# Optimization experiments

Measured on AMD Instinct MI355X. Metric: run time of the kernel, lower is better.

The kernel has to match this reference:

```python
import jax, jax.numpy as jnp
import numpy as np

E, N, D, H, K, S = 800000, 50000, 96, 8, 12, 32  # edges, nodes, dim, heads, head_dim, edge_scalar_dim


def smooth_leaky_relu(x, a=0.2):
    # equiformer SmoothLeakyReLU: (1+a)/2 * x + (1-a)/2 * x * (2*sigmoid(x) - 1)
    return ((1 + a) / 2) * x + ((1 - a) / 2) * x * (2 * jax.nn.sigmoid(x) - 1)


def setup_inputs() -> dict:
    key = jax.random.key(0)
    ks = jax.random.split(key, 16)
    inv = lambda n: 1.0 / np.sqrt(n)
    return {
        "message": jax.random.normal(ks[0], (E, D), jnp.float32),
        "edge_attr": jax.random.normal(ks[1], (E, 1), jnp.float32),
        "edge_scalars": jax.random.normal(ks[2], (E, S), jnp.float32),
        "W_rad1": jax.random.normal(ks[3], (S, S), jnp.float32) * inv(S),
        "b_rad1": jnp.zeros((S,), jnp.float32),
        "W_rad2": jax.random.normal(ks[4], (S, D), jnp.float32) * inv(S),
        "b_rad2": jnp.zeros((D,), jnp.float32),
        "W_alpha": jax.random.normal(ks[5], (D, D), jnp.float32) * inv(D),
        "W_lin": jax.random.normal(ks[6], (D, D), jnp.float32) * inv(D),
        "w_dtp2": jax.random.normal(ks[7], (D,), jnp.float32),
        "W_lin2": jax.random.normal(ks[8], (D, D), jnp.float32) * inv(D),
        "alpha_dot": jax.random.normal(ks[9], (H, K), jnp.float32) * inv(K),
        "W_proj": jax.random.normal(ks[10], (D, D), jnp.float32) * inv(D),
        "edge_dst": jnp.sort(jax.random.randint(ks[11], (E,), 0, N)),
        "n_nodes_dst": N,
    }


def reference(message, edge_attr, edge_scalars, W_rad1, b_rad1, W_rad2, b_rad2,
              W_alpha, W_lin, w_dtp2, W_lin2, alpha_dot, W_proj,
              edge_dst, n_nodes_dst):
    # sep_act.dtp_rad: radial MLP on edge scalars -> depthwise TP weights [E, D]
    weight = jax.nn.silu(edge_scalars @ W_rad1 + b_rad1) @ W_rad2 + b_rad2
    # sep_act.dtp: depthwise tensor product (scalar irreps -> per-channel product)
    msg = message * edge_attr * weight                      # [E, D]
    # sep_alpha: LinearRS to mul_alpha scalars, split into heads
    log_alpha = (msg @ W_alpha).reshape(E, H, K)            # [E, H, K]
    # sep_act.lin + gate (scalar gate == SiLU)
    value = jax.nn.silu(msg @ W_lin)                        # [E, D]
    # sep_value: internal-weight depthwise TP + linear
    value = (value * edge_attr * w_dtp2) @ W_lin2           # [E, D]
    # attention logits
    la = smooth_leaky_relu(log_alpha)
    logits = jnp.einsum('ehk,hk->eh', la, alpha_dot)        # [E, H]
    # scatter_logsumexp over destination nodes (segment softmax)
    m = jax.ops.segment_max(logits, edge_dst, num_segments=n_nodes_dst)     # [N, H]
    z = jax.ops.segment_sum(jnp.exp(logits - m[edge_dst]), edge_dst,
                            num_segments=n_nodes_dst)
    log_Z = m + jnp.log(z)                                  # [N, H]
    alpha = jnp.exp(logits - log_Z[edge_dst])               # [E, H]
    # weighted scatter-sum aggregation
    attn = jax.ops.segment_sum(value.reshape(E, H, K) * alpha[:, :, None],
                               edge_dst, num_segments=n_nodes_dst)          # [N, H, K]
    # heads2vec + proj
    return attn.reshape(n_nodes_dst, D) @ W_proj            # [N, D]
```

## Files before the change

kernel.cpp:

```cpp
#include <hip/hip_runtime.h>
#include <hip/hip_bf16.h>
#include <math.h>

#define D 96
#define H 8
#define KH 12
#define S 32

typedef __attribute__((ext_vector_type(8))) short short8;
typedef __attribute__((ext_vector_type(4))) float f32x4;

#define MFMA(a, b, c) __builtin_amdgcn_mfma_f32_16x16x32_bf16(a, b, c, 0, 0, 0)

__device__ __forceinline__ float sigmoidf_(float x) { return 1.0f / (1.0f + __expf(-x)); }
__device__ __forceinline__ float siluf_(float x) { return x * sigmoidf_(x); }
__device__ __forceinline__ float slrelu_(float x) {
    float s = sigmoidf_(x);
    return 0.6f * x + 0.4f * x * (2.0f * s - 1.0f);
}
__device__ __forceinline__ short f2bf(float f) {
    unsigned int u = __float_as_uint(f);
    u += 0x7fffu + ((u >> 16) & 1u);
    return (short)(u >> 16);
}
__device__ __forceinline__ float bf2f(ushort u) {
    return __uint_as_float(((unsigned int)u) << 16);
}

__global__ void pack_weights_kernel(
    const float* __restrict__ W1, const float* __restrict__ W2,
    const float* __restrict__ WA, const float* __restrict__ WL,
    const float* __restrict__ WL2, const float* __restrict__ WP,
    short* __restrict__ wB)
{
    int tid = blockIdx.x * 256 + threadIdx.x;
    if (tid >= 80 * 512) return;
    int j    = tid & 7;
    int lane = (tid >> 3) & 63;
    int fi   = tid >> 9;
    int q = lane >> 4, ln = lane & 15;
    const float* src; int ncols, tt, ff;
    if (fi < 2)       { src = W1;  ncols = 32; tt = fi;            ff = 0; }
    else if (fi < 8)  { src = W2;  ncols = 96; tt = fi - 2;        ff = 0; }
    else if (fi < 26) { src = WA;  ncols = 96; tt = (fi - 8) / 3;  ff = (fi - 8) % 3; }
    else if (fi < 44) { src = WL;  ncols = 96; tt = (fi - 26) / 3; ff = (fi - 26) % 3; }
    else if (fi < 62) { src = WL2; ncols = 96; tt = (fi - 44) / 3; ff = (fi - 44) % 3; }
    else              { src = WP;  ncols = 96; tt = (fi - 62) / 3; ff = (fi - 62) % 3; }
    int k = ff * 32 + q * 8 + j;
    int n = tt * 16 + ln;
    wB[tid] = f2bf(src[k * ncols + n]);
}

__global__ __launch_bounds__(256) void rowptr_kernel(
    const int* __restrict__ dst, int* __restrict__ rp, int E, int N)
{
    int e = blockIdx.x * 256 + threadIdx.x;
    if (e >= E) return;
    int cur  = dst[e];
    int prev = (e == 0) ? -1 : dst[e - 1];
    for (int n = prev + 1; n <= cur; n++) rp[n] = e;
    if (e == E - 1)
        for (int n = cur + 1; n <= N; n++) rp[n] = E;
}

__global__ __launch_bounds__(256, 6) void fused_edge_kernel(
    const float* __restrict__ message, const float* __restrict__ ea,
    const float* __restrict__ xs,
    const float* __restrict__ b1, const float* __restrict__ b2,
    const float* __restrict__ wdtp2, const float* __restrict__ adot,
    const short* __restrict__ wB,
    ushort* __restrict__ value, float* __restrict__ logits, int E)
{
    __shared__ __align__(16) char uni[64 * 97 * 4];
    short* sB = (short*)uni;
    float* sS = (float*)uni;
    const short8* wB8 = (const short8*)wB;

    const int t    = threadIdx.x;
    const int lane = t & 63;
    const int w    = t >> 6;
    const int q    = lane >> 4;
    const int ln   = lane & 15;
    const int row0 = blockIdx.x * 64;

    const int mA = w * 16 + ln;
    const int gA = row0 + mA;
    const int mC = w * 16 + q * 4;

    short8 af;
    {
        float4 x0 = make_float4(0, 0, 0, 0), x1 = x0;
        if (gA < E) {
            const float4* p = (const float4*)&xs[(size_t)gA * S + q * 8];
            x0 = p[0]; x1 = p[1];
        }
        af[0] = f2bf(x0.x); af[1] = f2bf(x0.y); af[2] = f2bf(x0.z); af[3] = f2bf(x0.w);
        af[4] = f2bf(x1.x); af[5] = f2bf(x1.y); af[6] = f2bf(x1.z); af[7] = f2bf(x1.w);
    }
    {
        f32x4 h0 = {0, 0, 0, 0}, h1 = {0, 0, 0, 0};
        h0 = MFMA(af, wB8[0 * 64 + lane], h0);
        h1 = MFMA(af, wB8[1 * 64 + lane], h1);
#pragma unroll
        for (int r = 0; r < 4; r++) {
            sB[(mC + r) * 104 + ln]      = f2bf(siluf_(h0[r] + b1[ln]));
            sB[(mC + r) * 104 + 16 + ln] = f2bf(siluf_(h1[r] + b1[16 + ln]));
        }
    }

    f32x4 acc[6];
    {
        short8 hf = *(const short8*)&sB[mA * 104 + q * 8];
#pragma unroll
        for (int i = 0; i < 6; i++) acc[i] = (f32x4){0, 0, 0, 0};
#pragma unroll
        for (int i = 0; i < 6; i++) acc[i] = MFMA(hf, wB8[(2 + i) * 64 + lane], acc[i]);
    }
    float eaR[4];
#pragma unroll
    for (int r = 0; r < 4; r++) {
        int gm = row0 + mC + r;
        eaR[r] = (gm < E) ? ea[gm] : 0.0f;
    }
#pragma unroll
    for (int i = 0; i < 6; i++) {
        int n = i * 16 + ln;
#pragma unroll
        for (int r = 0; r < 4; r++) {
            int gm = row0 + mC + r;
            float mv = (gm < E) ? message[(size_t)gm * D + n] : 0.0f;
            sB[(mC + r) * 104 + n] = f2bf(mv * eaR[r] * (acc[i][r] + b2[n]));
        }
    }

    short8 mf0 = *(const short8*)&sB[mA * 104 + 0  + q * 8];
    short8 mf1 = *(const short8*)&sB[mA * 104 + 32 + q * 8];
    short8 mf2 = *(const short8*)&sB[mA * 104 + 64 + q * 8];
    __syncthreads();

#pragma unroll
    for (int i = 0; i < 6; i++) acc[i] = (f32x4){0, 0, 0, 0};
#pragma unroll
    for (int i = 0; i < 6; i++) {
        acc[i] = MFMA(mf0, wB8[(8 + i * 3 + 0) * 64 + lane], acc[i]);
        acc[i] = MFMA(mf1, wB8[(8 + i * 3 + 1) * 64 + lane], acc[i]);
        acc[i] = MFMA(mf2, wB8[(8 + i * 3 + 2) * 64 + lane], acc[i]);
    }
#pragma unroll
    for (int i = 0; i < 6; i++) {
        int n = i * 16 + ln;
#pragma unroll
        for (int r = 0; r < 4; r++)
            sS[(mC + r) * 97 + n] = slrelu_(acc[i][r]);
    }
    __syncthreads();
    {
        int e = t & 63;
        int gm = row0 + e;
#pragma unroll
        for (int hh = 0; hh < 2; hh++) {
            int h = (t >> 6) * 2 + hh;
            float lg = 0.0f;
#pragma unroll
            for (int k = 0; k < KH; k++)
                lg += sS[e * 97 + h * KH + k] * adot[h * KH + k];
            if (gm < E) logits[(size_t)gm * H + h] = lg;
        }
    }
    __syncthreads();

#pragma unroll
    for (int i = 0; i < 6; i++) acc[i] = (f32x4){0, 0, 0, 0};
#pragma unroll
    for (int i = 0; i < 6; i++) {
        acc[i] = MFMA(mf0, wB8[(26 + i * 3 + 0) * 64 + lane], acc[i]);
        acc[i] = MFMA(mf1, wB8[(26 + i * 3 + 1) * 64 + lane], acc[i]);
        acc[i] = MFMA(mf2, wB8[(26 + i * 3 + 2) * 64 + lane], acc[i]);
    }
#pragma unroll
    for (int i = 0; i < 6; i++) {
        int n = i * 16 + ln;
#pragma unroll
        for (int r = 0; r < 4; r++)
            sB[(mC + r) * 104 + n] = f2bf(siluf_(acc[i][r]) * eaR[r] * wdtp2[n]);
    }

    {
        short8 vf0 = *(const short8*)&sB[mA * 104 + 0  + q * 8];
        short8 vf1 = *(const short8*)&sB[mA * 104 + 32 + q * 8];
        short8 vf2 = *(const short8*)&sB[mA * 104 + 64 + q * 8];
#pragma unroll
        for (int i = 0; i < 6; i++) acc[i] = (f32x4){0, 0, 0, 0};
#pragma unroll
        for (int i = 0; i < 6; i++) {
            acc[i] = MFMA(vf0, wB8[(44 + i * 3 + 0) * 64 + lane], acc[i]);
            acc[i] = MFMA(vf1, wB8[(44 + i * 3 + 1) * 64 + lane], acc[i]);
            acc[i] = MFMA(vf2, wB8[(44 + i * 3 + 2) * 64 + lane], acc[i]);
        }
#pragma unroll
        for (int i = 0; i < 6; i++) {
            int n = i * 16 + ln;
#pragma unroll
            for (int r = 0; r < 4; r++) {
                int gm = row0 + mC + r;
                if (gm < E) value[(size_t)gm * D + n] = (ushort)f2bf(acc[i][r]);
            }
        }
    }
}

__global__ __launch_bounds__(256) void logz_alpha_kernel(
    const float* __restrict__ logits, const int* __restrict__ rp,
    float* __restrict__ alphaU, float* __restrict__ zinv, int N)
{
    int tid = blockIdx.x * 256 + threadIdx.x;
    if (tid >= N * H) return;
    int n = tid >> 3, h = tid & 7;
    int s = rp[n], e1 = rp[n + 1];
    float m = -INFINITY;
    for (int e = s; e < e1; e++) m = fmaxf(m, logits[(size_t)e * H + h]);
    float z = 0.0f;
    for (int e = s; e < e1; e++) {
        float a = __expf(logits[(size_t)e * H + h] - m);
        z += a;
        alphaU[(size_t)e * H + h] = a;
    }
    zinv[tid] = (z > 0.0f) ? (1.0f / z) : 0.0f;
}

__global__ __launch_bounds__(256) void aggregate_kernel(
    const ushort* __restrict__ value, const float* __restrict__ alphaU,
    const float* __restrict__ zinv, const int* __restrict__ rp,
    ushort* __restrict__ attnB, int N)
{
    int tid = blockIdx.x * 256 + threadIdx.x;
    if (tid >= N * 24) return;
    int n = tid / 24, g = tid % 24;
    int d0 = g * 4, h = g / 3;
    int s = rp[n], e1 = rp[n + 1];
    const char* vb = (const char*)value;
    float a0 = 0.0f, a1 = 0.0f, a2 = 0.0f, a3 = 0.0f;
    for (int e = s; e < e1; e++) {
        uint2 v = *(const uint2*)(vb + (size_t)e * 192 + d0 * 2);
        float a = alphaU[(size_t)e * H + h];
        a0 += __uint_as_float(v.x << 16) * a;
        a1 += __uint_as_float(v.x & 0xffff0000u) * a;
        a2 += __uint_as_float(v.y << 16) * a;
        a3 += __uint_as_float(v.y & 0xffff0000u) * a;
    }
    float zi = zinv[n * H + h];
    ushort4 o;
    o.x = (ushort)f2bf(a0 * zi);
    o.y = (ushort)f2bf(a1 * zi);
    o.z = (ushort)f2bf(a2 * zi);
    o.w = (ushort)f2bf(a3 * zi);
    *(ushort4*)&attnB[(size_t)n * D + d0] = o;
}

__global__ __launch_bounds__(256) void proj_kernel(
    const ushort* __restrict__ attnB, const short* __restrict__ wB,
    float* __restrict__ out, int rows)
{
    const short8* wB8 = (const short8*)wB;
    const int t    = threadIdx.x;
    const int lane = t & 63;
    const int w    = t >> 6;
    const int q    = lane >> 4;
    const int ln   = lane & 15;
    const int row0 = blockIdx.x * 64;
    const int mA   = w * 16 + ln;
    const int gA   = row0 + mA;
    const int mC   = w * 16 + q * 4;

    short8 mf0 = {0,0,0,0,0,0,0,0}, mf1 = mf0, mf2 = mf0;
    if (gA < rows) {
        mf0 = *(const short8*)&attnB[(size_t)gA * D + 0  + q * 8];
        mf1 = *(const short8*)&attnB[(size_t)gA * D + 32 + q * 8];
        mf2 = *(const short8*)&attnB[(size_t)gA * D + 64 + q * 8];
    }
    f32x4 acc[6];
#pragma unroll
    for (int i = 0; i < 6; i++) acc[i] = (f32x4){0, 0, 0, 0};
#pragma unroll
    for (int i = 0; i < 6; i++) {
        acc[i] = MFMA(mf0, wB8[(62 + i * 3 + 0) * 64 + lane], acc[i]);
        acc[i] = MFMA(mf1, wB8[(62 + i * 3 + 1) * 64 + lane], acc[i]);
        acc[i] = MFMA(mf2, wB8[(62 + i * 3 + 2) * 64 + lane], acc[i]);
    }
#pragma unroll
    for (int i = 0; i < 6; i++) {
        int nn = i * 16 + ln;
#pragma unroll
        for (int r = 0; r < 4; r++) {
            int gm = row0 + mC + r;
            if (gm < rows) out[(size_t)gm * D + nn] = acc[i][r];
        }
    }
}

extern "C" void kernel_launch(void* const* d_in, const int* in_sizes, int n_in,
                              void* d_out, int out_size, void* d_ws, size_t ws_size,
                              hipStream_t stream)
{
    const float* message      = (const float*)d_in[0];
    const float* edge_attr    = (const float*)d_in[1];
    const float* edge_scalars = (const float*)d_in[2];
    const float* W_rad1       = (const float*)d_in[3];
    const float* b_rad1       = (const float*)d_in[4];
    const float* W_rad2       = (const float*)d_in[5];
    const float* b_rad2       = (const float*)d_in[6];
    const float* W_alpha      = (const float*)d_in[7];
    const float* W_lin        = (const float*)d_in[8];
    const float* w_dtp2       = (const float*)d_in[9];
    const float* W_lin2       = (const float*)d_in[10];
    const float* alpha_dot    = (const float*)d_in[11];
    const float* W_proj       = (const float*)d_in[12];
    const int*   edge_dst     = (const int*)d_in[13];
    float* out = (float*)d_out;

    const int E = in_sizes[0] / D;
    const int N = out_size / D;

    char* p = (char*)d_ws;
    ushort* value  = (ushort*)p;            p += (size_t)E * D * 2;
    float*  logits = (float*)p;             p += (size_t)E * H * 4;
    float*  alphaU = (float*)p;             p += (size_t)E * H * 4;
    float*  zinv   = (float*)p;             p += (size_t)N * H * 4;
    ushort* attnB  = (ushort*)p;            p += (size_t)N * D * 2;
    int*    rp     = (int*)p;               p += ((size_t)(N + 1) * 4 + 15) & ~(size_t)15;
    short*  wBuf   = (short*)p;

    pack_weights_kernel<<<(80 * 512 + 255) / 256, 256, 0, stream>>>(
        W_rad1, W_rad2, W_alpha, W_lin, W_lin2, W_proj, wBuf);
    rowptr_kernel<<<(E + 255) / 256, 256, 0, stream>>>(edge_dst, rp, E, N);
    fused_edge_kernel<<<(E + 63) / 64, 256, 0, stream>>>(
        message, edge_attr, edge_scalars, b_rad1, b_rad2, w_dtp2, alpha_dot,
        wBuf, value, logits, E);
    logz_alpha_kernel<<<(N * H + 255) / 256, 256, 0, stream>>>(logits, rp, alphaU, zinv, N);
    aggregate_kernel<<<(N * 24 + 255) / 256, 256, 0, stream>>>(value, alphaU, zinv, rp, attnB, N);
    proj_kernel<<<(N + 63) / 64, 256, 0, stream>>>(attnB, wBuf, out, N);
}
```

Measured before the change: 782.6 us.

## Make edge kernel warp-private and fuse softmax with aggregation into one node kernel

The edge kernel gives each wavefront its own LDS slice, so block-wide __syncthreads become per-wave LDS waitcnt fences. Tail handling switches to clamped indices, occupancy is raised to 8 blocks, and value is staged through LDS so it can be written with 16-byte stores. The separate logsumexp and aggregation kernels are merged into one wave-per-node kernel that recomputes exp on the fly, which removes the alphaU/zinv buffers and one launch. The cost is recomputing exp per channel and serial per-node loops that can leave lanes idle on skewed degrees.

Result: faster. 737.0 us (-5.8%).

```diff
diff --git a/kernel.cpp b/kernel.cpp
--- a/kernel.cpp
+++ b/kernel.cpp
@@ -1,5 +1,4 @@
 #include <hip/hip_runtime.h>
-#include <hip/hip_bf16.h>
 #include <math.h>
 
 #define D 96
@@ -15,8 +14,7 @@
 __device__ __forceinline__ float sigmoidf_(float x) { return 1.0f / (1.0f + __expf(-x)); }
 __device__ __forceinline__ float siluf_(float x) { return x * sigmoidf_(x); }
 __device__ __forceinline__ float slrelu_(float x) {
-    float s = sigmoidf_(x);
-    return 0.6f * x + 0.4f * x * (2.0f * s - 1.0f);
+    return x * (0.2f + 0.8f * sigmoidf_(x));
 }
 __device__ __forceinline__ short f2bf(float f) {
     unsigned int u = __float_as_uint(f);
@@ -26,6 +24,11 @@
 __device__ __forceinline__ float bf2f(ushort u) {
     return __uint_as_float(((unsigned int)u) << 16);
 }
+
+#define LDSFENCE() do { \
+    asm volatile("s_waitcnt lgkmcnt(0)" ::: "memory"); \
+    __builtin_amdgcn_sched_barrier(0); \
+} while (0)
 
 __global__ void pack_weights_kernel(
     const float* __restrict__ W1, const float* __restrict__ W2,
@@ -63,7 +66,7 @@
         for (int n = cur + 1; n <= N; n++) rp[n] = E;
 }
 
-__global__ __launch_bounds__(256, 6) void fused_edge_kernel(
+__global__ __launch_bounds__(256, 8) void fused_edge_kernel(
     const float* __restrict__ message, const float* __restrict__ ea,
     const float* __restrict__ xs,
     const float* __restrict__ b1, const float* __restrict__ b2,
@@ -71,9 +74,7 @@
     const short* __restrict__ wB,
     ushort* __restrict__ value, float* __restrict__ logits, int E)
 {
-    __shared__ __align__(16) char uni[64 * 97 * 4];
-    short* sB = (short*)uni;
-    float* sS = (float*)uni;
+    __shared__ __align__(16) char uni[4][3328];
     const short8* wB8 = (const short8*)wB;
 
     const int t    = threadIdx.x;
@@ -81,62 +82,67 @@
     const int w    = t >> 6;
     const int q    = lane >> 4;
     const int ln   = lane & 15;
-    const int row0 = blockIdx.x * 64;
-
-    const int mA = w * 16 + ln;
-    const int gA = row0 + mA;
-    const int mC = w * 16 + q * 4;
-
-    short8 af;
+    const int row0 = blockIdx.x * 64 + w * 16;
+
+    short* sB = (short*)(uni[w]);
+    float* sS = (float*)(uni[w]);
+
+    const int Ec = E - 1;
+    const int gA = min(row0 + ln, Ec);
+    const int rA = ln;
+    const int rC = q * 4;
+
+    float eaR[4];
+    int   gCc[4];
+    bool  okC[4];
+#pragma unroll
+    for (int r = 0; r < 4; r++) {
+        int g  = row0 + rC + r;
+        okC[r] = (g < E);
+        gCc[r] = min(g, Ec);
+        eaR[r] = ea[gCc[r]];
+    }
+
     {
-        float4 x0 = make_float4(0, 0, 0, 0), x1 = x0;
-        if (gA < E) {
-            const float4* p = (const float4*)&xs[(size_t)gA * S + q * 8];
-            x0 = p[0]; x1 = p[1];
-        }
+        const float4* p = (const float4*)&xs[(size_t)gA * S + q * 8];
+        float4 x0 = p[0], x1 = p[1];
+        short8 af;
         af[0] = f2bf(x0.x); af[1] = f2bf(x0.y); af[2] = f2bf(x0.z); af[3] = f2bf(x0.w);
         af[4] = f2bf(x1.x); af[5] = f2bf(x1.y); af[6] = f2bf(x1.z); af[7] = f2bf(x1.w);
-    }
-    {
         f32x4 h0 = {0, 0, 0, 0}, h1 = {0, 0, 0, 0};
         h0 = MFMA(af, wB8[0 * 64 + lane], h0);
         h1 = MFMA(af, wB8[1 * 64 + lane], h1);
+        float bb0 = b1[ln], bb1 = b1[16 + ln];
 #pragma unroll
         for (int r = 0; r < 4; r++) {
-            sB[(mC + r) * 104 + ln]      = f2bf(siluf_(h0[r] + b1[ln]));
-            sB[(mC + r) * 104 + 16 + ln] = f2bf(siluf_(h1[r] + b1[16 + ln]));
+            sB[(rC + r) * 104 + ln]      = f2bf(siluf_(h0[r] + bb0));
+            sB[(rC + r) * 104 + 16 + ln] = f2bf(siluf_(h1[r] + bb1));
         }
     }
 
     f32x4 acc[6];
     {
-        short8 hf = *(const short8*)&sB[mA * 104 + q * 8];
+        short8 hf = *(const short8*)&sB[rA * 104 + q * 8];
 #pragma unroll
         for (int i = 0; i < 6; i++) acc[i] = (f32x4){0, 0, 0, 0};
 #pragma unroll
         for (int i = 0; i < 6; i++) acc[i] = MFMA(hf, wB8[(2 + i) * 64 + lane], acc[i]);
     }
-    float eaR[4];
-#pragma unroll
-    for (int r = 0; r < 4; r++) {
-        int gm = row0 + mC + r;
-        eaR[r] = (gm < E) ? ea[gm] : 0.0f;
-    }
 #pragma unroll
     for (int i = 0; i < 6; i++) {
         int n = i * 16 + ln;
+        float bb = b2[n];
 #pragma unroll
         for (int r = 0; r < 4; r++) {
-            int gm = row0 + mC + r;
-            float mv = (gm < E) ? message[(size_t)gm * D + n] : 0.0f;
-            sB[(mC + r) * 104 + n] = f2bf(mv * eaR[r] * (acc[i][r] + b2[n]));
-        }
-    }
-
-    short8 mf0 = *(const short8*)&sB[mA * 104 + 0  + q * 8];
-    short8 mf1 = *(const short8*)&sB[mA * 104 + 32 + q * 8];
-    short8 mf2 = *(const short8*)&sB[mA * 104 + 64 + q * 8];
-    __syncthreads();
+            float mv = message[(size_t)gCc[r] * D + n];
+            sB[(rC + r) * 104 + n] = f2bf(mv * eaR[r] * (acc[i][r] + bb));
+        }
+    }
+
+    short8 mf0 = *(const short8*)&sB[rA * 104 + 0  + q * 8];
+    short8 mf1 = *(const short8*)&sB[rA * 104 + 32 + q * 8];
+    short8 mf2 = *(const short8*)&sB[rA * 104 + 64 + q * 8];
+    LDSFENCE();
 
 #pragma unroll
     for (int i = 0; i < 6; i++) acc[i] = (f32x4){0, 0, 0, 0};
@@ -146,28 +152,28 @@
         acc[i] = MFMA(mf1, wB8[(8 + i * 3 + 1) * 64 + lane], acc[i]);
         acc[i] = MFMA(mf2, wB8[(8 + i * 3 + 2) * 64 + lane], acc[i]);
     }
-#pragma unroll
-    for (int i = 0; i < 6; i++) {
-        int n = i * 16 + ln;
-#pragma unroll
-        for (int r = 0; r < 4; r++)
-            sS[(mC + r) * 97 + n] = slrelu_(acc[i][r]);
-    }
-    __syncthreads();
     {
-        int e = t & 63;
-        int gm = row0 + e;
-#pragma unroll
-        for (int hh = 0; hh < 2; hh++) {
-            int h = (t >> 6) * 2 + hh;
+        const int rloc = lane >> 2, hh = lane & 3;
+        const int gm = row0 + rloc;
+        const bool ok = (gm < E);
+#pragma unroll
+        for (int half = 0; half < 2; half++) {
+#pragma unroll
+            for (int i = 0; i < 3; i++) {
+                int ii = half * 3 + i;
+#pragma unroll
+                for (int r = 0; r < 4; r++)
+                    sS[(rC + r) * 50 + i * 16 + ln] = slrelu_(acc[ii][r]);
+            }
+            int h = half * 4 + hh;
             float lg = 0.0f;
 #pragma unroll
             for (int k = 0; k < KH; k++)
-                lg += sS[e * 97 + h * KH + k] * adot[h * KH + k];
-            if (gm < E) logits[(size_t)gm * H + h] = lg;
-        }
-    }
-    __syncthreads();
+                lg += sS[rloc * 50 + hh * KH + k] * adot[h * KH + k];
+            if (ok) logits[(size_t)gm * H + h] = lg;
+        }
+    }
+    LDSFENCE();
 
 #pragma unroll
     for (int i = 0; i < 6; i++) acc[i] = (f32x4){0, 0, 0, 0};
@@ -180,15 +186,16 @@
 #pragma unroll
     for (int i = 0; i < 6; i++) {
         int n = i * 16 + ln;
+        float wd = wdtp2[n];
 #pragma unroll
         for (int r = 0; r < 4; r++)
-            sB[(mC + r) * 104 + n] = f2bf(siluf_(acc[i][r]) * eaR[r] * wdtp2[n]);
+            sB[(rC + r) * 104 + n] = f2bf(siluf_(acc[i][r]) * eaR[r] * wd);
     }
 
     {
-        short8 vf0 = *(const short8*)&sB[mA * 104 + 0  + q * 8];
-        short8 vf1 = *(const short8*)&sB[mA * 104 + 32 + q * 8];
-        short8 vf2 = *(const short8*)&sB[mA * 104 + 64 + q * 8];
+        short8 vf0 = *(const short8*)&sB[rA * 104 + 0  + q * 8];
+        short8 vf1 = *(const short8*)&sB[rA * 104 + 32 + q * 8];
+        short8 vf2 = *(const short8*)&sB[rA * 104 + 64 + q * 8];
 #pragma unroll
         for (int i = 0; i < 6; i++) acc[i] = (f32x4){0, 0, 0, 0};
 #pragma unroll
@@ -201,60 +208,62 @@
         for (int i = 0; i < 6; i++) {
             int n = i * 16 + ln;
 #pragma unroll
-            for (int r = 0; r < 4; r++) {
-                int gm = row0 + mC + r;
-                if (gm < E) value[(size_t)gm * D + n] = (ushort)f2bf(acc[i][r]);
+            for (int r = 0; r < 4; r++)
+                sB[(rC + r) * 104 + n] = f2bf(acc[i][r]);
+        }
+        const int rloc = lane >> 2, c0 = lane & 3;
+        const int gm = row0 + rloc;
+        if (gm < E) {
+#pragma unroll
+            for (int j = 0; j < 3; j++) {
+                short8 v = *(const short8*)&sB[rloc * 104 + (c0 + 4 * j) * 8];
+                *(short8*)&value[(size_t)gm * D + (c0 + 4 * j) * 8] = v;
             }
         }
     }
 }
 
-__global__ __launch_bounds__(256) void logz_alpha_kernel(
-    const float* __restrict__ logits, const int* __restrict__ rp,
-    float* __restrict__ alphaU, float* __restrict__ zinv, int N)
-{
-    int tid = blockIdx.x * 256 + threadIdx.x;
-    if (tid >= N * H) return;
-    int n = tid >> 3, h = tid & 7;
-    int s = rp[n], e1 = rp[n + 1];
+__global__ __launch_bounds__(256) void node_kernel(
+    const float* __restrict__ logits, const ushort* __restrict__ value,
+    const int* __restrict__ rp, ushort* __restrict__ attnB, int N)
+{
+    const int wid  = (blockIdx.x * 256 + threadIdx.x) >> 6;
+    const int lane = threadIdx.x & 63;
+    if (wid >= N) return;
+    const int s  = rp[wid];
+    const int e1 = rp[wid + 1];
+
+    const int h = lane & 7, eo = lane >> 3;
     float m = -INFINITY;
-    for (int e = s; e < e1; e++) m = fmaxf(m, logits[(size_t)e * H + h]);
+    for (int e = s + eo; e < e1; e += 8)
+        m = fmaxf(m, logits[(size_t)e * H + h]);
+    m = fmaxf(m, __shfl_xor(m, 8));
+    m = fmaxf(m, __shfl_xor(m, 16));
+    m = fmaxf(m, __shfl_xor(m, 32));
     float z = 0.0f;
-    for (int e = s; e < e1; e++) {
-        float a = __expf(logits[(size_t)e * H + h] - m);
-        z += a;
-        alphaU[(size_t)e * H + h] = a;
-    }
-    zinv[tid] = (z > 0.0f) ? (1.0f / z) : 0.0f;
-}
-
-__global__ __launch_bounds__(256) void aggregate_kernel(
-    const ushort* __restrict__ value, const float* __restrict__ alphaU,
-    const float* __restrict__ zinv, const int* __restrict__ rp,
-    ushort* __restrict__ attnB, int N)
-{
-    int tid = blockIdx.x * 256 + threadIdx.x;
-    if (tid >= N * 24) return;
-    int n = tid / 24, g = tid % 24;
-    int d0 = g * 4, h = g / 3;
-    int s = rp[n], e1 = rp[n + 1];
-    const char* vb = (const char*)value;
-    float a0 = 0.0f, a1 = 0.0f, a2 = 0.0f, a3 = 0.0f;
-    for (int e = s; e < e1; e++) {
-        uint2 v = *(const uint2*)(vb + (size_t)e * 192 + d0 * 2);
-        float a = alphaU[(size_t)e * H + h];
-        a0 += __uint_as_float(v.x << 16) * a;
-        a1 += __uint_as_float(v.x & 0xffff0000u) * a;
-        a2 += __uint_as_float(v.y << 16) * a;
-        a3 += __uint_as_float(v.y & 0xffff0000u) * a;
-    }
-    float zi = zinv[n * H + h];
-    ushort4 o;
-    o.x = (ushort)f2bf(a0 * zi);
-    o.y = (ushort)f2bf(a1 * zi);
-    o.z = (ushort)f2bf(a2 * zi);
-    o.w = (ushort)f2bf(a3 * zi);
-    *(ushort4*)&attnB[(size_t)n * D + d0] = o;
+    for (int e = s + eo; e < e1; e += 8)
+        z += __expf(logits[(size_t)e * H + h] - m);
+    z += __shfl_xor(z, 8);
+    z += __shfl_xor(z, 16);
+    z += __shfl_xor(z, 32);
+
+    if (lane < 48) {
+        const int   hc  = lane / 6;
+        const float mh  = __shfl(m, hc);
+        const float zv  = __shfl(z, hc);
+        const float zih = (zv > 0.0f) ? (1.0f / zv) : 0.0f;
+        const int c = 2 * lane;
+        float a0 = 0.0f, a1 = 0.0f;
+        for (int e = s; e < e1; e++) {
+            float a = __expf(logits[(size_t)e * H + hc] - mh);
+            unsigned v = *(const unsigned*)&value[(size_t)e * D + c];
+            a0 += __uint_as_float(v << 16) * a;
+            a1 += __uint_as_float(v & 0xffff0000u) * a;
+        }
+        unsigned lo = (unsigned)(ushort)f2bf(a0 * zih);
+        unsigned hi = (unsigned)(ushort)f2bf(a1 * zih);
+        *(unsigned*)&attnB[(size_t)wid * D + c] = lo | (hi << 16);
+    }
 }
 
 __global__ __launch_bounds__(256) void proj_kernel(
@@ -272,7 +281,7 @@
     const int gA   = row0 + mA;
     const int mC   = w * 16 + q * 4;
 
-    short8 mf0 = {0,0,0,0,0,0,0,0}, mf1 = mf0, mf2 = mf0;
+    short8 mf0 = {0, 0, 0, 0, 0, 0, 0, 0}, mf1 = mf0, mf2 = mf0;
     if (gA < rows) {
         mf0 = *(const short8*)&attnB[(size_t)gA * D + 0  + q * 8];
         mf1 = *(const short8*)&attnB[(size_t)gA * D + 32 + q * 8];
@@ -322,12 +331,10 @@
     const int N = out_size / D;
 
     char* p = (char*)d_ws;
-    ushort* value  = (ushort*)p;            p += (size_t)E * D * 2;
-    float*  logits = (float*)p;             p += (size_t)E * H * 4;
-    float*  alphaU = (float*)p;             p += (size_t)E * H * 4;
-    float*  zinv   = (float*)p;             p += (size_t)N * H * 4;
-    ushort* attnB  = (ushort*)p;            p += (size_t)N * D * 2;
-    int*    rp     = (int*)p;               p += ((size_t)(N + 1) * 4 + 15) & ~(size_t)15;
+    ushort* value  = (ushort*)p;  p += (size_t)E * D * 2;
+    float*  logits = (float*)p;   p += (size_t)E * H * 4;
+    ushort* attnB  = (ushort*)p;  p += ((size_t)N * D * 2 + 15) & ~(size_t)15;
+    int*    rp     = (int*)p;     p += ((size_t)(N + 1) * 4 + 15) & ~(size_t)15;
     short*  wBuf   = (short*)p;
 
     pack_weights_kernel<<<(80 * 512 + 255) / 256, 256, 0, stream>>>(
@@ -336,7 +343,6 @@
     fused_edge_kernel<<<(E + 63) / 64, 256, 0, stream>>>(
         message, edge_attr, edge_scalars, b_rad1, b_rad2, w_dtp2, alpha_dot,
         wBuf, value, logits, E);
-    logz_alpha_kernel<<<(N * H + 255) / 256, 256, 0, stream>>>(logits, rp, alphaU, zinv, N);
-    aggregate_kernel<<<(N * 24 + 255) / 256, 256, 0, stream>>>(value, alphaU, zinv, rp, attnB, N);
+    node_kernel<<<(N + 3) / 4, 256, 0, stream>>>(logits, value, rp, attnB, N);
     proj_kernel<<<(N + 63) / 64, 256, 0, stream>>>(attnB, wBuf, out, N);
 }
```
